# Kernel tuning notes

Hardware: AMD Instinct MI355X
Metric: run time of the kernel (lower is better)

The kernel has to match this reference:

```python
import jax, jax.numpy as jnp
import numpy as np

B, L, D = 8, 1024, 512
H, DK, DV = 8, 64, 64
DLAT = 512

def _ln(x, g, b, eps):
    m = jnp.mean(x, axis=-1, keepdims=True)
    var = jnp.mean((x - m) ** 2, axis=-1, keepdims=True)
    return (x - m) * jax.lax.rsqrt(var + eps) * g + b

def setup_inputs() -> dict:
    key = jax.random.key(0)
    ks = jax.random.split(key, 16)
    s = lambda fan: 1.0 / np.sqrt(fan)
    inp = {
        "q": jax.random.normal(ks[0], (B, L, D), jnp.float32),
        "k": jax.random.normal(ks[1], (B, L, D), jnp.float32),
        "v": jax.random.normal(ks[2], (B, L, D), jnp.float32),
        "latent": jax.random.normal(ks[3], (B, 1, DLAT), jnp.float32),
        "Wq": jax.random.normal(ks[4], (D, H * DK), jnp.float32) * s(D),
        "bq": jnp.zeros((H * DK,), jnp.float32),
        "Wk": jax.random.normal(ks[5], (D, H * DK), jnp.float32) * s(D),
        "bk": jnp.zeros((H * DK,), jnp.float32),
        "Wv": jax.random.normal(ks[6], (D, H * DV), jnp.float32) * s(D),
        "bv": jnp.zeros((H * DV,), jnp.float32),
        "Wfc": jax.random.normal(ks[7], (H * DV, D), jnp.float32) * s(H * DV),
        "bfc": jnp.zeros((D,), jnp.float32),
        "Ws1": jax.random.normal(ks[8], (DLAT, 2 * D), jnp.float32) * s(DLAT),
        "bs1": jnp.zeros((2 * D,), jnp.float32),
        "Ws2": jax.random.normal(ks[9], (D, D), jnp.float32) * s(D),
        "bs2": jnp.zeros((D,), jnp.float32),
        "en_g": jnp.ones((D,), jnp.float32),
        "en_b": jnp.zeros((D,), jnp.float32),
        "ln_g": jnp.ones((D,), jnp.float32),
        "ln_b": jnp.zeros((D,), jnp.float32),
    }
    return inp

def reference(q, k, v, latent, Wq, bq, Wk, bk, Wv, bv, Wfc, bfc, Ws1, bs1, Ws2, bs2, en_g, en_b, ln_g, ln_b):
    residual = q
    # QKV projections -> [B, L, H, d]
    Q = (q @ Wq + bq).reshape(B, L, H, DK)
    K = (k @ Wk + bk).reshape(B, L, H, DK)
    V = (v @ Wv + bv).reshape(B, L, H, DV)
    # scaled dot-product attention (dropout = identity in eval)
    scores = jnp.einsum("bqhd,bkhd->bhqk", Q, K) / jnp.sqrt(jnp.float32(DK))
    attn = jax.nn.softmax(scores, axis=-1)
    o = jnp.einsum("bhqk,bkhd->bqhd", attn, V).reshape(B, L, H * DV)
    o = o @ Wfc + bfc
    # ScaledStylizationBlock (FiLM): SiLU -> Linear -> split scale/shift
    lat = jax.nn.silu(latent) @ Ws1 + bs1          # [B, 1, 2D]
    scale, shift = jnp.split(lat, 2, axis=2)
    h = _ln(o, en_g, en_b, 1e-5) * (1.0 + scale) + shift
    h = jax.nn.silu(h) @ Ws2 + bs2
    out = _ln(h + residual, ln_g, ln_b, 1e-6)
    return out, attn
```

## Files before the change

kernel.cpp:

```cpp
#include <hip/hip_runtime.h>
#include <hip/hip_bf16.h>
#include <math.h>

#define BB 8
#define LLEN 1024
#define DDIM 512
#define HH 8
#define DLAT 512
#define NROW (BB * LLEN)
#define ROWELEM 4194304

typedef __bf16 bf16x8 __attribute__((ext_vector_type(8)));
typedef __bf16 bf16x4 __attribute__((ext_vector_type(4)));
typedef float  f32x4  __attribute__((ext_vector_type(4)));

__device__ inline __bf16 f2bf(float f) {
    union { float f; unsigned u; } a; a.f = f;
    unsigned r = (a.u + 0x7fffu + ((a.u >> 16) & 1u)) >> 16;
    union { unsigned short s; __bf16 b; } o; o.s = (unsigned short)r;
    return o.b;
}

__global__ __launch_bounds__(256) void wtrans3_kernel(
    const float* __restrict__ W0, const float* __restrict__ W1,
    const float* __restrict__ W2, __bf16* __restrict__ T0,
    __bf16* __restrict__ T1, __bf16* __restrict__ T2)
{
    const float* W = (blockIdx.y == 0) ? W0 : (blockIdx.y == 1) ? W1 : W2;
    __bf16* WT     = (blockIdx.y == 0) ? T0 : (blockIdx.y == 1) ? T1 : T2;

    __shared__ float t[64][65];
    const int tid = threadIdx.x;
    const int bx = blockIdx.x & 7;
    const int by = blockIdx.x >> 3;
    const int r0 = by * 64, c0 = bx * 64;

    #pragma unroll
    for (int p = 0; p < 4; ++p) {
        int r = p * 16 + (tid >> 4);
        int c = (tid & 15) * 4;
        f32x4 v = *(const f32x4*)(W + (size_t)(r0 + r) * 512 + c0 + c);
        t[r][c] = v[0]; t[r][c + 1] = v[1]; t[r][c + 2] = v[2]; t[r][c + 3] = v[3];
    }
    __syncthreads();
    #pragma unroll
    for (int p = 0; p < 4; ++p) {
        int c = p * 16 + (tid >> 4);
        int rc = (tid & 15) * 4;
        bf16x4 o;
        #pragma unroll
        for (int m = 0; m < 4; ++m) o[m] = f2bf(t[rc + m][c]);
        *(bf16x4*)(WT + (size_t)(c0 + c) * 512 + r0 + rc) = o;
    }
}

__global__ __launch_bounds__(256) void wtrans_hilo2_kernel(
    const float* __restrict__ W0, const float* __restrict__ W1,
    __bf16* __restrict__ H0, __bf16* __restrict__ L0,
    __bf16* __restrict__ H1, __bf16* __restrict__ L1)
{
    const float* W  = (blockIdx.y == 0) ? W0 : W1;
    __bf16* WTh     = (blockIdx.y == 0) ? H0 : H1;
    __bf16* WTl     = (blockIdx.y == 0) ? L0 : L1;

    __shared__ float t[64][65];
    const int tid = threadIdx.x;
    const int bx = blockIdx.x & 7;
    const int by = blockIdx.x >> 3;
    const int r0 = by * 64, c0 = bx * 64;

    #pragma unroll
    for (int p = 0; p < 4; ++p) {
        int r = p * 16 + (tid >> 4);
        int c = (tid & 15) * 4;
        f32x4 v = *(const f32x4*)(W + (size_t)(r0 + r) * 512 + c0 + c);
        t[r][c] = v[0]; t[r][c + 1] = v[1]; t[r][c + 2] = v[2]; t[r][c + 3] = v[3];
    }
    __syncthreads();
    #pragma unroll
    for (int p = 0; p < 4; ++p) {
        int c = p * 16 + (tid >> 4);
        int rc = (tid & 15) * 4;
        bf16x4 oh, ol;
        #pragma unroll
        for (int m = 0; m < 4; ++m) {
            float v = t[rc + m][c];
            __bf16 hi = f2bf(v);
            oh[m] = hi;
            ol[m] = f2bf(v - (float)hi);
        }
        *(bf16x4*)(WTh + (size_t)(c0 + c) * 512 + r0 + rc) = oh;
        *(bf16x4*)(WTl + (size_t)(c0 + c) * 512 + r0 + rc) = ol;
    }
}

__global__ __launch_bounds__(256) void gemm_qkv_mfma(
    const float* __restrict__ A, const __bf16* __restrict__ Bt,
    const float* __restrict__ bias, __bf16* __restrict__ C)
{
    const int tid  = threadIdx.x;
    const int w    = tid >> 6, lane = tid & 63;
    const int quad = lane >> 4, lid = lane & 15;
    const int wm = w >> 1, wn = w & 1;
    const int col0 = blockIdx.x * 64;
    const int row0 = blockIdx.y * 128;

    __shared__ __bf16 As[128][72];
    __shared__ __bf16 Bs[64][72];

    const f32x4 zero = {0.f, 0.f, 0.f, 0.f};
    f32x4 acc[4][2];
    #pragma unroll
    for (int i = 0; i < 4; ++i)
        #pragma unroll
        for (int j = 0; j < 2; ++j) acc[i][j] = zero;

    for (int kt = 0; kt < 512; kt += 64) {
        __syncthreads();
        {
            const int rr = lane >> 4;
            const int cc = lane & 15;
            #pragma unroll
            for (int p = 0; p < 8; ++p) {
                int r = w * 32 + p * 4 + rr;
                f32x4 v = *(const f32x4*)(A + (size_t)(row0 + r) * 512 + kt + cc * 4);
                bf16x4 o;
                #pragma unroll
                for (int m = 0; m < 4; ++m) o[m] = f2bf(v[m]);
                *(bf16x4*)&As[r][cc * 4] = o;
            }
        }
        {
            const int rr = lane >> 3;
            const int cc = lane & 7;
            #pragma unroll
            for (int p = 0; p < 2; ++p) {
                int r = w * 16 + p * 8 + rr;
                *(bf16x8*)&Bs[r][cc * 8] =
                    *(const bf16x8*)(Bt + (size_t)(col0 + r) * 512 + kt + cc * 8);
            }
        }
        __syncthreads();
        #pragma unroll
        for (int ks = 0; ks < 2; ++ks) {
            bf16x8 a[4], b[2];
            #pragma unroll
            for (int i = 0; i < 4; ++i)
                a[i] = *(const bf16x8*)&As[wm * 64 + i * 16 + lid][ks * 32 + quad * 8];
            #pragma unroll
            for (int j = 0; j < 2; ++j)
                b[j] = *(const bf16x8*)&Bs[wn * 32 + j * 16 + lid][ks * 32 + quad * 8];
            #pragma unroll
            for (int i = 0; i < 4; ++i)
                #pragma unroll
                for (int j = 0; j < 2; ++j)
                    acc[i][j] = __builtin_amdgcn_mfma_f32_16x16x32_bf16(a[i], b[j], acc[i][j], 0, 0, 0);
        }
    }

    float bcol[2];
    #pragma unroll
    for (int j = 0; j < 2; ++j) bcol[j] = bias[col0 + wn * 32 + j * 16 + lid];
    #pragma unroll
    for (int i = 0; i < 4; ++i)
        #pragma unroll
        for (int j = 0; j < 2; ++j) {
            int colg = col0 + wn * 32 + j * 16 + lid;
            #pragma unroll
            for (int r = 0; r < 4; ++r) {
                int rowg = row0 + wm * 64 + i * 16 + quad * 4 + r;
                C[(size_t)rowg * 512 + colg] = f2bf(acc[i][j][r] + bcol[j]);
            }
        }
}

__global__ __launch_bounds__(256) void gemm_v_mfma(
    const float* __restrict__ A, const __bf16* __restrict__ Bt,
    const float* __restrict__ bias, __bf16* __restrict__ VtG)
{
    const int tid  = threadIdx.x;
    const int w    = tid >> 6, lane = tid & 63;
    const int quad = lane >> 4, lid = lane & 15;
    const int wm = w >> 1, wn = w & 1;
    const int col0 = blockIdx.x * 64;
    const int row0 = blockIdx.y * 128;

    __shared__ __bf16 As[128][72];
    __shared__ __bf16 Bs[64][72];

    const f32x4 zero = {0.f, 0.f, 0.f, 0.f};
    f32x4 acc[4][2];
    #pragma unroll
    for (int i = 0; i < 4; ++i)
        #pragma unroll
        for (int j = 0; j < 2; ++j) acc[i][j] = zero;

    for (int kt = 0; kt < 512; kt += 64) {
        __syncthreads();
        {
            const int rr = lane >> 4;
            const int cc = lane & 15;
            #pragma unroll
            for (int p = 0; p < 8; ++p) {
                int r = w * 32 + p * 4 + rr;
                f32x4 v = *(const f32x4*)(A + (size_t)(row0 + r) * 512 + kt + cc * 4);
                bf16x4 o;
                #pragma unroll
                for (int m = 0; m < 4; ++m) o[m] = f2bf(v[m]);
                *(bf16x4*)&As[r][cc * 4] = o;
            }
        }
        {
            const int rr = lane >> 3;
            const int cc = lane & 7;
            #pragma unroll
            for (int p = 0; p < 2; ++p) {
                int r = w * 16 + p * 8 + rr;
                *(bf16x8*)&Bs[r][cc * 8] =
                    *(const bf16x8*)(Bt + (size_t)(col0 + r) * 512 + kt + cc * 8);
            }
        }
        __syncthreads();
        #pragma unroll
        for (int ks = 0; ks < 2; ++ks) {
            bf16x8 a[4], b[2];
            #pragma unroll
            for (int i = 0; i < 4; ++i)
                a[i] = *(const bf16x8*)&As[wm * 64 + i * 16 + lid][ks * 32 + quad * 8];
            #pragma unroll
            for (int j = 0; j < 2; ++j)
                b[j] = *(const bf16x8*)&Bs[wn * 32 + j * 16 + lid][ks * 32 + quad * 8];
            #pragma unroll
            for (int i = 0; i < 4; ++i)
                #pragma unroll
                for (int j = 0; j < 2; ++j)
                    acc[i][j] = __builtin_amdgcn_mfma_f32_16x16x32_bf16(a[i], b[j], acc[i][j], 0, 0, 0);
        }
    }

    __syncthreads();
    __bf16 (*Ts)[136] = (__bf16 (*)[136])(&As[0][0]);
    float bcol[2];
    #pragma unroll
    for (int j = 0; j < 2; ++j) bcol[j] = bias[col0 + wn * 32 + j * 16 + lid];
    #pragma unroll
    for (int i = 0; i < 4; ++i)
        #pragma unroll
        for (int j = 0; j < 2; ++j) {
            int d = wn * 32 + j * 16 + lid;
            #pragma unroll
            for (int r = 0; r < 4; ++r) {
                int l = wm * 64 + i * 16 + quad * 4 + r;
                Ts[d][l] = f2bf(acc[i][j][r] + bcol[j]);
            }
        }
    __syncthreads();
    const int b = row0 >> 10, l0 = row0 & 1023, h = blockIdx.x;
    const size_t obase = (size_t)((b * 8 + h) * 64) * LLEN;
    #pragma unroll
    for (int p = 0; p < 4; ++p) {
        int cix = tid + p * 256;
        int d = cix >> 4, lc = cix & 15;
        bf16x8 vv = *(const bf16x8*)&Ts[d][lc * 8];
        *(bf16x8*)(VtG + obase + (size_t)d * LLEN + l0 + lc * 8) = vv;
    }
}

__global__ __launch_bounds__(256) void gemm_split_mfma(
    const __bf16* __restrict__ Ahi, const __bf16* __restrict__ Alo,
    const __bf16* __restrict__ Bth, const __bf16* __restrict__ Btl,
    const float* __restrict__ bias, float* __restrict__ C)
{
    const int tid  = threadIdx.x;
    const int w    = tid >> 6, lane = tid & 63;
    const int quad = lane >> 4, lid = lane & 15;
    const int wm = w >> 1, wn = w & 1;
    const int col0 = blockIdx.x * 64;
    const int row0 = blockIdx.y * 128;

    __shared__ __bf16 Ah[128][40];
    __shared__ __bf16 Al[128][40];
    __shared__ __bf16 Bh[64][40];
    __shared__ __bf16 Bl[64][40];

    const f32x4 zero = {0.f, 0.f, 0.f, 0.f};
    f32x4 acc[4][2];
    #pragma unroll
    for (int i = 0; i < 4; ++i)
        #pragma unroll
        for (int j = 0; j < 2; ++j) acc[i][j] = zero;

    for (int kt = 0; kt < 512; kt += 32) {
        __syncthreads();
        #pragma unroll
        for (int p = 0; p < 2; ++p) {
            int cix = tid + p * 256;
            int r = cix >> 2, cc = cix & 3;
            size_t g = (size_t)(row0 + r) * 512 + kt + cc * 8;
            *(bf16x8*)&Ah[r][cc * 8] = *(const bf16x8*)(Ahi + g);
            *(bf16x8*)&Al[r][cc * 8] = *(const bf16x8*)(Alo + g);
        }
        {
            int r = tid >> 2, cc = tid & 3;
            size_t g = (size_t)(col0 + r) * 512 + kt + cc * 8;
            *(bf16x8*)&Bh[r][cc * 8] = *(const bf16x8*)(Bth + g);
            *(bf16x8*)&Bl[r][cc * 8] = *(const bf16x8*)(Btl + g);
        }
        __syncthreads();
        bf16x8 ah[4], al[4], bh[2], bl[2];
        #pragma unroll
        for (int i = 0; i < 4; ++i) {
            ah[i] = *(const bf16x8*)&Ah[wm * 64 + i * 16 + lid][quad * 8];
            al[i] = *(const bf16x8*)&Al[wm * 64 + i * 16 + lid][quad * 8];
        }
        #pragma unroll
        for (int j = 0; j < 2; ++j) {
            bh[j] = *(const bf16x8*)&Bh[wn * 32 + j * 16 + lid][quad * 8];
            bl[j] = *(const bf16x8*)&Bl[wn * 32 + j * 16 + lid][quad * 8];
        }
        #pragma unroll
        for (int i = 0; i < 4; ++i)
            #pragma unroll
            for (int j = 0; j < 2; ++j) {
                f32x4 t = __builtin_amdgcn_mfma_f32_16x16x32_bf16(al[i], bh[j], acc[i][j], 0, 0, 0);
                t = __builtin_amdgcn_mfma_f32_16x16x32_bf16(ah[i], bl[j], t, 0, 0, 0);
                acc[i][j] = __builtin_amdgcn_mfma_f32_16x16x32_bf16(ah[i], bh[j], t, 0, 0, 0);
            }
    }

    float bcol[2];
    #pragma unroll
    for (int j = 0; j < 2; ++j) bcol[j] = bias[col0 + wn * 32 + j * 16 + lid];
    #pragma unroll
    for (int i = 0; i < 4; ++i)
        #pragma unroll
        for (int j = 0; j < 2; ++j) {
            int colg = col0 + wn * 32 + j * 16 + lid;
            #pragma unroll
            for (int r = 0; r < 4; ++r) {
                int rowg = row0 + wm * 64 + i * 16 + quad * 4 + r;
                C[(size_t)rowg * 512 + colg] = acc[i][j][r] + bcol[j];
            }
        }
}

__global__ __launch_bounds__(256) void film_latent_kernel(
    const float* __restrict__ latent, const float* __restrict__ Ws1,
    const float* __restrict__ bs1, float* __restrict__ film)
{
    __shared__ float sl[DLAT];
    const int b = blockIdx.x;
    const int tid = threadIdx.x;
    #pragma unroll
    for (int l = 0; l < 2; ++l) {
        int k = tid + l * 256;
        float x = latent[b * DLAT + k];
        sl[k] = x / (1.f + __expf(-x));
    }
    __syncthreads();
    int n = blockIdx.y * 256 + tid;
    float acc = bs1[n];
    for (int k = 0; k < DLAT; ++k)
        acc += sl[k] * Ws1[(size_t)k * 1024 + n];
    film[b * 1024 + n] = acc;
}

__global__ __launch_bounds__(256) void attn_mfma_kernel(
    const __bf16* __restrict__ Qb, const __bf16* __restrict__ Kb,
    const __bf16* __restrict__ VtG, float* __restrict__ attn_out,
    __bf16* __restrict__ Ohi, __bf16* __restrict__ Olo)
{
    const int bid = blockIdx.x;
    const int qt = bid & 15;
    const int h  = (bid >> 4) & 7;
    const int b  = bid >> 7;
    const int q0 = qt * 64;
    const int tid = threadIdx.x;
    const int w    = tid >> 6;
    const int lane = tid & 63;
    const int quad = lane >> 4;
    const int lid  = lane & 15;

    __shared__ __bf16 KtS[2][64][72];
    __shared__ __bf16 VtS[2][64][72];
    __shared__ __bf16 PtS[4][16][72];

    const int myq = q0 + w * 16 + lid;
    const __bf16* qptr = Qb + (size_t)(b * LLEN + myq) * DDIM + h * 64 + quad * 8;
    const bf16x8 qf0 = *(const bf16x8*)(qptr);
    const bf16x8 qf1 = *(const bf16x8*)(qptr + 32);

    const size_t kbase = (size_t)(b * LLEN) * DDIM + h * 64;
    const size_t vbase = (size_t)((b * 8 + h) * 64) * LLEN;
    const f32x4 zero = {0.f, 0.f, 0.f, 0.f};
    const float C0 = 0.125f;

    const int sr = tid >> 3;
    const int sc = tid & 7;

    #pragma unroll
    for (int rep = 0; rep < 2; ++rep) {
        int r = sr + rep * 32;
        *(bf16x8*)&KtS[0][r][sc * 8] =
            *(const bf16x8*)(Kb + kbase + (size_t)r * DDIM + sc * 8);
    }
    __syncthreads();

    float rsum = 0.f;
    int cur = 0;
    for (int kt = 0; kt < 16; ++kt) {
        bf16x8 kr0, kr1;
        if (kt < 15) {
            kr0 = *(const bf16x8*)(Kb + kbase + (size_t)((kt + 1) * 64 + sr) * DDIM + sc * 8);
            kr1 = *(const bf16x8*)(Kb + kbase + (size_t)((kt + 1) * 64 + sr + 32) * DDIM + sc * 8);
        }
        #pragma unroll
        for (int st = 0; st < 4; ++st) {
            bf16x8 a0 = *(const bf16x8*)&KtS[cur][st * 16 + lid][quad * 8];
            bf16x8 a1 = *(const bf16x8*)&KtS[cur][st * 16 + lid][32 + quad * 8];
            f32x4 c = __builtin_amdgcn_mfma_f32_16x16x32_bf16(a0, qf0, zero, 0, 0, 0);
            c = __builtin_amdgcn_mfma_f32_16x16x32_bf16(a1, qf1, c, 0, 0, 0);
            #pragma unroll
            for (int r = 0; r < 4; ++r) rsum += __expf(C0 * c[r]);
        }
        if (kt < 15) {
            *(bf16x8*)&KtS[cur ^ 1][sr][sc * 8] = kr0;
            *(bf16x8*)&KtS[cur ^ 1][sr + 32][sc * 8] = kr1;
        }
        __syncthreads();
        cur ^= 1;
    }
    rsum += __shfl_xor(rsum, 16, 64);
    rsum += __shfl_xor(rsum, 32, 64);
    const float rinv = 1.f / rsum;

    f32x4 oacc[4] = {zero, zero, zero, zero};
    const size_t abase = ((size_t)((b * 8 + h) * LLEN + myq)) * LLEN;

    #pragma unroll
    for (int rep = 0; rep < 2; ++rep) {
        int r = sr + rep * 32;
        *(bf16x8*)&KtS[0][r][sc * 8] =
            *(const bf16x8*)(Kb + kbase + (size_t)r * DDIM + sc * 8);
        *(bf16x8*)&VtS[0][r][sc * 8] =
            *(const bf16x8*)(VtG + vbase + (size_t)r * LLEN + sc * 8);
    }
    __syncthreads();

    cur = 0;
    for (int kt = 0; kt < 16; ++kt) {
        bf16x8 kr0, kr1, vr0, vr1;
        if (kt < 15) {
            kr0 = *(const bf16x8*)(Kb + kbase + (size_t)((kt + 1) * 64 + sr) * DDIM + sc * 8);
            kr1 = *(const bf16x8*)(Kb + kbase + (size_t)((kt + 1) * 64 + sr + 32) * DDIM + sc * 8);
            vr0 = *(const bf16x8*)(VtG + vbase + (size_t)sr * LLEN + (kt + 1) * 64 + sc * 8);
            vr1 = *(const bf16x8*)(VtG + vbase + (size_t)(sr + 32) * LLEN + (kt + 1) * 64 + sc * 8);
        }
        #pragma unroll
        for (int st = 0; st < 4; ++st) {
            bf16x8 a0 = *(const bf16x8*)&KtS[cur][st * 16 + lid][quad * 8];
            bf16x8 a1 = *(const bf16x8*)&KtS[cur][st * 16 + lid][32 + quad * 8];
            f32x4 c = __builtin_amdgcn_mfma_f32_16x16x32_bf16(a0, qf0, zero, 0, 0, 0);
            c = __builtin_amdgcn_mfma_f32_16x16x32_bf16(a1, qf1, c, 0, 0, 0);
            f32x4 p;
            bf16x4 pk;
            #pragma unroll
            for (int r = 0; r < 4; ++r) {
                p[r] = __expf(C0 * c[r]) * rinv;
                pk[r] = f2bf(p[r]);
            }
            __builtin_nontemporal_store(p, (f32x4*)(attn_out + abase + kt * 64 + st * 16 + quad * 4));
            *(bf16x4*)&PtS[w][lid][st * 16 + quad * 4] = pk;
        }
        asm volatile("s_waitcnt lgkmcnt(0)" ::: "memory");
        #pragma unroll
        for (int kc = 0; kc < 2; ++kc) {
            bf16x8 pa = *(const bf16x8*)&PtS[w][lid][kc * 32 + quad * 8];
            #pragma unroll
            for (int nt = 0; nt < 4; ++nt) {
                bf16x8 vb = *(const bf16x8*)&VtS[cur][nt * 16 + lid][kc * 32 + quad * 8];
                oacc[nt] = __builtin_amdgcn_mfma_f32_16x16x32_bf16(pa, vb, oacc[nt], 0, 0, 0);
            }
        }
        if (kt < 15) {
            *(bf16x8*)&KtS[cur ^ 1][sr][sc * 8] = kr0;
            *(bf16x8*)&KtS[cur ^ 1][sr + 32][sc * 8] = kr1;
            *(bf16x8*)&VtS[cur ^ 1][sr][sc * 8] = vr0;
            *(bf16x8*)&VtS[cur ^ 1][sr + 32][sc * 8] = vr1;
        }
        __syncthreads();
        cur ^= 1;
    }

    #pragma unroll
    for (int nt = 0; nt < 4; ++nt)
        #pragma unroll
        for (int r = 0; r < 4; ++r) {
            float val = oacc[nt][r];
            __bf16 hi = f2bf(val);
            size_t idx = (size_t)(b * LLEN + q0 + w * 16 + quad * 4 + r) * DDIM + h * 64 + nt * 16 + lid;
            Ohi[idx] = hi;
            Olo[idx] = f2bf(val - (float)hi);
        }
}

__device__ inline void block_reduce2(float& a, float& b) {
    #pragma unroll
    for (int off = 32; off > 0; off >>= 1) {
        a += __shfl_down(a, off, 64);
        b += __shfl_down(b, off, 64);
    }
    __shared__ float wa[4], wb[4];
    int lane = threadIdx.x & 63, w = threadIdx.x >> 6;
    if (lane == 0) { wa[w] = a; wb[w] = b; }
    __syncthreads();
    if (threadIdx.x == 0) {
        wa[0] = wa[0] + wa[1] + wa[2] + wa[3];
        wb[0] = wb[0] + wb[1] + wb[2] + wb[3];
    }
    __syncthreads();
    a = wa[0];
    b = wb[0];
}

__global__ __launch_bounds__(256) void film_ln_kernel(
    const float* __restrict__ X, const float* __restrict__ en_g,
    const float* __restrict__ en_b, const float* __restrict__ film,
    __bf16* __restrict__ HShi, __bf16* __restrict__ HSlo)
{
    const int row = blockIdx.x;
    const int b = row >> 10;
    const int tid = threadIdx.x;
    const size_t base = (size_t)row * DDIM;

    float x0 = X[base + tid];
    float x1 = X[base + 256 + tid];
    float s = x0 + x1;
    float s2 = x0 * x0 + x1 * x1;
    block_reduce2(s, s2);
    float mean = s * (1.f / 512.f);
    float var = s2 * (1.f / 512.f) - mean * mean;
    float inv = rsqrtf(var + 1e-5f);

    #pragma unroll
    for (int l = 0; l < 2; ++l) {
        int d = tid + l * 256;
        float x = (l == 0) ? x0 : x1;
        float nh = (x - mean) * inv * en_g[d] + en_b[d];
        float sc = film[b * 1024 + d];
        float sh = film[b * 1024 + 512 + d];
        float hv = nh * (1.f + sc) + sh;
        float sv = hv / (1.f + __expf(-hv));
        __bf16 hi = f2bf(sv);
        HShi[base + d] = hi;
        HSlo[base + d] = f2bf(sv - (float)hi);
    }
}

__global__ __launch_bounds__(256) void final_ln_kernel(
    const float* __restrict__ H2, const float* __restrict__ resid,
    const float* __restrict__ g, const float* __restrict__ bta,
    float* __restrict__ out)
{
    const int row = blockIdx.x;
    const int tid = threadIdx.x;
    const size_t base = (size_t)row * DDIM;

    float x0 = H2[base + tid] + resid[base + tid];
    float x1 = H2[base + 256 + tid] + resid[base + 256 + tid];
    float s = x0 + x1;
    float s2 = x0 * x0 + x1 * x1;
    block_reduce2(s, s2);
    float mean = s * (1.f / 512.f);
    float var = s2 * (1.f / 512.f) - mean * mean;
    float inv = rsqrtf(var + 1e-6f);

    #pragma unroll
    for (int l = 0; l < 2; ++l) {
        int d = tid + l * 256;
        float x = (l == 0) ? x0 : x1;
        float o = (x - mean) * inv * g[d] + bta[d];
        __builtin_nontemporal_store(o, out + base + d);
    }
}

extern "C" void kernel_launch(void* const* d_in, const int* in_sizes, int n_in,
                              void* d_out, int out_size, void* d_ws, size_t ws_size,
                              hipStream_t stream)
{
    const float* q      = (const float*)d_in[0];
    const float* k      = (const float*)d_in[1];
    const float* v      = (const float*)d_in[2];
    const float* latent = (const float*)d_in[3];
    const float* Wq  = (const float*)d_in[4];
    const float* bq  = (const float*)d_in[5];
    const float* Wk  = (const float*)d_in[6];
    const float* bk  = (const float*)d_in[7];
    const float* Wv  = (const float*)d_in[8];
    const float* bv  = (const float*)d_in[9];
    const float* Wfc = (const float*)d_in[10];
    const float* bfc = (const float*)d_in[11];
    const float* Ws1 = (const float*)d_in[12];
    const float* bs1 = (const float*)d_in[13];
    const float* Ws2 = (const float*)d_in[14];
    const float* bs2 = (const float*)d_in[15];
    const float* en_g = (const float*)d_in[16];
    const float* en_b = (const float*)d_in[17];
    const float* ln_g = (const float*)d_in[18];
    const float* ln_b = (const float*)d_in[19];

    float* out  = (float*)d_out;
    float* attn = out + ROWELEM;

    char* ws = (char*)d_ws;
    __bf16* Qb   = (__bf16*)(ws + 0);
    __bf16* Kb   = (__bf16*)(ws + 8388608);
    __bf16* VtG  = (__bf16*)(ws + 16777216);
    __bf16* Ohi  = (__bf16*)(ws + 25165824);
    __bf16* Olo  = (__bf16*)(ws + 33554432);
    __bf16* WqT  = (__bf16*)(ws + 41943040);
    __bf16* WkT  = (__bf16*)(ws + 42467328);
    __bf16* WvT  = (__bf16*)(ws + 42991616);
    __bf16* WfhT = (__bf16*)(ws + 43515904);
    __bf16* WflT = (__bf16*)(ws + 44040192);
    __bf16* W2hT = (__bf16*)(ws + 44564480);
    __bf16* W2lT = (__bf16*)(ws + 45088768);
    float*  film = (float*)(ws + 45613056);

    float*  F1   = (float*)(ws + 0);
    __bf16* HShi = Ohi;
    __bf16* HSlo = Olo;
    float*  H2   = (float*)(ws + 0);

    wtrans3_kernel<<<dim3(64, 3), 256, 0, stream>>>(Wq, Wk, Wv, WqT, WkT, WvT);
    wtrans_hilo2_kernel<<<dim3(64, 2), 256, 0, stream>>>(Wfc, Ws2, WfhT, WflT, W2hT, W2lT);
    film_latent_kernel<<<dim3(BB, 4), 256, 0, stream>>>(latent, Ws1, bs1, film);

    dim3 ggrid(8, 64);
    gemm_qkv_mfma<<<ggrid, 256, 0, stream>>>(q, WqT, bq, Qb);
    gemm_qkv_mfma<<<ggrid, 256, 0, stream>>>(k, WkT, bk, Kb);
    gemm_v_mfma<<<ggrid, 256, 0, stream>>>(v, WvT, bv, VtG);

    attn_mfma_kernel<<<1024, 256, 0, stream>>>(Qb, Kb, VtG, attn, Ohi, Olo);

    gemm_split_mfma<<<ggrid, 256, 0, stream>>>(Ohi, Olo, WfhT, WflT, bfc, F1);
    film_ln_kernel<<<NROW, 256, 0, stream>>>(F1, en_g, en_b, film, HShi, HSlo);
    gemm_split_mfma<<<ggrid, 256, 0, stream>>>(HShi, HSlo, W2hT, W2lT, bs2, H2);
    final_ln_kernel<<<NROW, 256, 0, stream>>>(H2, q, ln_g, ln_b, out);
}
```

Before: 578.4 us.

## Merge weight prep and QKV GEMMs, shrink split-GEMM tiles, remap blocks across XCDs

Folds the two weight-transpose kernels into one launch and the three Q/K/V projection GEMMs into a single 1536-block launch. Halves the row tile of the hi/lo split GEMM to 64 so 1024 blocks fill the GPU. Adds an XCD-aware block index permutation (f&7 stride) to the attention, QKV and split GEMM kernels so neighbouring tiles land on the same chiplet and share L2. The intent is fewer launches, better occupancy and better cache locality, at the cost of smaller tiles with less operand reuse in the split GEMM.

```diff
diff --git a/kernel.cpp b/kernel.cpp
--- a/kernel.cpp
+++ b/kernel.cpp
@@ -21,13 +21,22 @@
     return o.b;
 }
 
-__global__ __launch_bounds__(256) void wtrans3_kernel(
-    const float* __restrict__ W0, const float* __restrict__ W1,
-    const float* __restrict__ W2, __bf16* __restrict__ T0,
-    __bf16* __restrict__ T1, __bf16* __restrict__ T2)
-{
-    const float* W = (blockIdx.y == 0) ? W0 : (blockIdx.y == 1) ? W1 : W2;
-    __bf16* WT     = (blockIdx.y == 0) ? T0 : (blockIdx.y == 1) ? T1 : T2;
+__global__ __launch_bounds__(256) void wprep_kernel(
+    const float* __restrict__ Wq, const float* __restrict__ Wk,
+    const float* __restrict__ Wv, const float* __restrict__ Wfc,
+    const float* __restrict__ Ws2,
+    __bf16* __restrict__ WqT, __bf16* __restrict__ WkT, __bf16* __restrict__ WvT,
+    __bf16* __restrict__ WfhT, __bf16* __restrict__ WflT,
+    __bf16* __restrict__ W2hT, __bf16* __restrict__ W2lT)
+{
+    const float* W; __bf16* D0; __bf16* D1 = nullptr;
+    switch (blockIdx.y) {
+        case 0: W = Wq;  D0 = WqT;  break;
+        case 1: W = Wk;  D0 = WkT;  break;
+        case 2: W = Wv;  D0 = WvT;  break;
+        case 3: W = Wfc; D0 = WfhT; D1 = WflT; break;
+        default: W = Ws2; D0 = W2hT; D1 = W2lT; break;
+    }
 
     __shared__ float t[64][65];
     const int tid = threadIdx.x;
@@ -47,63 +56,52 @@
     for (int p = 0; p < 4; ++p) {
         int c = p * 16 + (tid >> 4);
         int rc = (tid & 15) * 4;
-        bf16x4 o;
-        #pragma unroll
-        for (int m = 0; m < 4; ++m) o[m] = f2bf(t[rc + m][c]);
-        *(bf16x4*)(WT + (size_t)(c0 + c) * 512 + r0 + rc) = o;
-    }
-}
-
-__global__ __launch_bounds__(256) void wtrans_hilo2_kernel(
-    const float* __restrict__ W0, const float* __restrict__ W1,
-    __bf16* __restrict__ H0, __bf16* __restrict__ L0,
-    __bf16* __restrict__ H1, __bf16* __restrict__ L1)
-{
-    const float* W  = (blockIdx.y == 0) ? W0 : W1;
-    __bf16* WTh     = (blockIdx.y == 0) ? H0 : H1;
-    __bf16* WTl     = (blockIdx.y == 0) ? L0 : L1;
-
-    __shared__ float t[64][65];
-    const int tid = threadIdx.x;
-    const int bx = blockIdx.x & 7;
-    const int by = blockIdx.x >> 3;
-    const int r0 = by * 64, c0 = bx * 64;
-
-    #pragma unroll
-    for (int p = 0; p < 4; ++p) {
-        int r = p * 16 + (tid >> 4);
-        int c = (tid & 15) * 4;
-        f32x4 v = *(const f32x4*)(W + (size_t)(r0 + r) * 512 + c0 + c);
-        t[r][c] = v[0]; t[r][c + 1] = v[1]; t[r][c + 2] = v[2]; t[r][c + 3] = v[3];
-    }
-    __syncthreads();
-    #pragma unroll
-    for (int p = 0; p < 4; ++p) {
-        int c = p * 16 + (tid >> 4);
-        int rc = (tid & 15) * 4;
-        bf16x4 oh, ol;
-        #pragma unroll
-        for (int m = 0; m < 4; ++m) {
-            float v = t[rc + m][c];
-            __bf16 hi = f2bf(v);
-            oh[m] = hi;
-            ol[m] = f2bf(v - (float)hi);
-        }
-        *(bf16x4*)(WTh + (size_t)(c0 + c) * 512 + r0 + rc) = oh;
-        *(bf16x4*)(WTl + (size_t)(c0 + c) * 512 + r0 + rc) = ol;
-    }
-}
-
-__global__ __launch_bounds__(256) void gemm_qkv_mfma(
-    const float* __restrict__ A, const __bf16* __restrict__ Bt,
-    const float* __restrict__ bias, __bf16* __restrict__ C)
-{
+        if (D1 == nullptr) {
+            bf16x4 o;
+            #pragma unroll
+            for (int m = 0; m < 4; ++m) o[m] = f2bf(t[rc + m][c]);
+            *(bf16x4*)(D0 + (size_t)(c0 + c) * 512 + r0 + rc) = o;
+        } else {
+            bf16x4 oh, ol;
+            #pragma unroll
+            for (int m = 0; m < 4; ++m) {
+                float v = t[rc + m][c];
+                __bf16 hi = f2bf(v);
+                oh[m] = hi;
+                ol[m] = f2bf(v - (float)hi);
+            }
+            *(bf16x4*)(D0 + (size_t)(c0 + c) * 512 + r0 + rc) = oh;
+            *(bf16x4*)(D1 + (size_t)(c0 + c) * 512 + r0 + rc) = ol;
+        }
+    }
+}
+
+__global__ __launch_bounds__(256) void gemm_qkv3_mfma(
+    const float* __restrict__ q, const float* __restrict__ k,
+    const float* __restrict__ v,
+    const __bf16* __restrict__ WqT, const __bf16* __restrict__ WkT,
+    const __bf16* __restrict__ WvT,
+    const float* __restrict__ bq, const float* __restrict__ bk,
+    const float* __restrict__ bv,
+    __bf16* __restrict__ Qb, __bf16* __restrict__ Kb, __bf16* __restrict__ VtG)
+{
+    const int f = blockIdx.x;
+    const int s = (f & 7) * 192 + (f >> 3);
+    const int z   = s >> 9;
+    const int rem = s & 511;
+    const int bx  = rem & 7;
+    const int by  = rem >> 3;
+
+    const float*  A    = (z == 0) ? q   : (z == 1) ? k   : v;
+    const __bf16* Bt   = (z == 0) ? WqT : (z == 1) ? WkT : WvT;
+    const float*  bias = (z == 0) ? bq  : (z == 1) ? bk  : bv;
+
     const int tid  = threadIdx.x;
     const int w    = tid >> 6, lane = tid & 63;
     const int quad = lane >> 4, lid = lane & 15;
     const int wm = w >> 1, wn = w & 1;
-    const int col0 = blockIdx.x * 64;
-    const int row0 = blockIdx.y * 128;
+    const int col0 = bx * 64;
+    const int row0 = by * 128;
 
     __shared__ __bf16 As[128][72];
     __shared__ __bf16 Bs[64][72];
@@ -123,10 +121,10 @@
             #pragma unroll
             for (int p = 0; p < 8; ++p) {
                 int r = w * 32 + p * 4 + rr;
-                f32x4 v = *(const f32x4*)(A + (size_t)(row0 + r) * 512 + kt + cc * 4);
+                f32x4 vv = *(const f32x4*)(A + (size_t)(row0 + r) * 512 + kt + cc * 4);
                 bf16x4 o;
                 #pragma unroll
-                for (int m = 0; m < 4; ++m) o[m] = f2bf(v[m]);
+                for (int m = 0; m < 4; ++m) o[m] = f2bf(vv[m]);
                 *(bf16x4*)&As[r][cc * 4] = o;
             }
         }
@@ -161,157 +159,93 @@
     float bcol[2];
     #pragma unroll
     for (int j = 0; j < 2; ++j) bcol[j] = bias[col0 + wn * 32 + j * 16 + lid];
-    #pragma unroll
-    for (int i = 0; i < 4; ++i)
-        #pragma unroll
-        for (int j = 0; j < 2; ++j) {
-            int colg = col0 + wn * 32 + j * 16 + lid;
-            #pragma unroll
-            for (int r = 0; r < 4; ++r) {
-                int rowg = row0 + wm * 64 + i * 16 + quad * 4 + r;
-                C[(size_t)rowg * 512 + colg] = f2bf(acc[i][j][r] + bcol[j]);
-            }
-        }
-}
-
-__global__ __launch_bounds__(256) void gemm_v_mfma(
-    const float* __restrict__ A, const __bf16* __restrict__ Bt,
-    const float* __restrict__ bias, __bf16* __restrict__ VtG)
-{
+
+    if (z < 2) {
+        __bf16* C = (z == 0) ? Qb : Kb;
+        #pragma unroll
+        for (int i = 0; i < 4; ++i)
+            #pragma unroll
+            for (int j = 0; j < 2; ++j) {
+                int colg = col0 + wn * 32 + j * 16 + lid;
+                #pragma unroll
+                for (int r = 0; r < 4; ++r) {
+                    int rowg = row0 + wm * 64 + i * 16 + quad * 4 + r;
+                    C[(size_t)rowg * 512 + colg] = f2bf(acc[i][j][r] + bcol[j]);
+                }
+            }
+    } else {
+        __syncthreads();
+        __bf16 (*Ts)[136] = (__bf16 (*)[136])(&As[0][0]);
+        #pragma unroll
+        for (int i = 0; i < 4; ++i)
+            #pragma unroll
+            for (int j = 0; j < 2; ++j) {
+                int d = wn * 32 + j * 16 + lid;
+                #pragma unroll
+                for (int r = 0; r < 4; ++r) {
+                    int l = wm * 64 + i * 16 + quad * 4 + r;
+                    Ts[d][l] = f2bf(acc[i][j][r] + bcol[j]);
+                }
+            }
+        __syncthreads();
+        const int b = row0 >> 10, l0 = row0 & 1023, h = bx;
+        const size_t obase = (size_t)((b * 8 + h) * 64) * LLEN;
+        #pragma unroll
+        for (int p = 0; p < 4; ++p) {
+            int cix = tid + p * 256;
+            int d = cix >> 4, lc = cix & 15;
+            bf16x8 vv = *(const bf16x8*)&Ts[d][lc * 8];
+            *(bf16x8*)(VtG + obase + (size_t)d * LLEN + l0 + lc * 8) = vv;
+        }
+    }
+}
+
+__global__ __launch_bounds__(256) void gemm_split_mfma(
+    const __bf16* __restrict__ Ahi, const __bf16* __restrict__ Alo,
+    const __bf16* __restrict__ Bth, const __bf16* __restrict__ Btl,
+    const float* __restrict__ bias, float* __restrict__ C)
+{
+    const int f = blockIdx.x;
+    const int s = (f & 7) * 128 + (f >> 3);
+    const int bx = s & 7, by = s >> 3;
+    const int col0 = bx * 64;
+    const int row0 = by * 64;
+
     const int tid  = threadIdx.x;
     const int w    = tid >> 6, lane = tid & 63;
     const int quad = lane >> 4, lid = lane & 15;
     const int wm = w >> 1, wn = w & 1;
-    const int col0 = blockIdx.x * 64;
-    const int row0 = blockIdx.y * 128;
-
-    __shared__ __bf16 As[128][72];
-    __shared__ __bf16 Bs[64][72];
-
-    const f32x4 zero = {0.f, 0.f, 0.f, 0.f};
-    f32x4 acc[4][2];
-    #pragma unroll
-    for (int i = 0; i < 4; ++i)
-        #pragma unroll
-        for (int j = 0; j < 2; ++j) acc[i][j] = zero;
-
-    for (int kt = 0; kt < 512; kt += 64) {
-        __syncthreads();
-        {
-            const int rr = lane >> 4;
-            const int cc = lane & 15;
-            #pragma unroll
-            for (int p = 0; p < 8; ++p) {
-                int r = w * 32 + p * 4 + rr;
-                f32x4 v = *(const f32x4*)(A + (size_t)(row0 + r) * 512 + kt + cc * 4);
-                bf16x4 o;
-                #pragma unroll
-                for (int m = 0; m < 4; ++m) o[m] = f2bf(v[m]);
-                *(bf16x4*)&As[r][cc * 4] = o;
-            }
-        }
-        {
-            const int rr = lane >> 3;
-            const int cc = lane & 7;
-            #pragma unroll
-            for (int p = 0; p < 2; ++p) {
-                int r = w * 16 + p * 8 + rr;
-                *(bf16x8*)&Bs[r][cc * 8] =
-                    *(const bf16x8*)(Bt + (size_t)(col0 + r) * 512 + kt + cc * 8);
-            }
-        }
-        __syncthreads();
-        #pragma unroll
-        for (int ks = 0; ks < 2; ++ks) {
-            bf16x8 a[4], b[2];
-            #pragma unroll
-            for (int i = 0; i < 4; ++i)
-                a[i] = *(const bf16x8*)&As[wm * 64 + i * 16 + lid][ks * 32 + quad * 8];
-            #pragma unroll
-            for (int j = 0; j < 2; ++j)
-                b[j] = *(const bf16x8*)&Bs[wn * 32 + j * 16 + lid][ks * 32 + quad * 8];
-            #pragma unroll
-            for (int i = 0; i < 4; ++i)
-                #pragma unroll
-                for (int j = 0; j < 2; ++j)
-                    acc[i][j] = __builtin_amdgcn_mfma_f32_16x16x32_bf16(a[i], b[j], acc[i][j], 0, 0, 0);
-        }
-    }
-
-    __syncthreads();
-    __bf16 (*Ts)[136] = (__bf16 (*)[136])(&As[0][0]);
-    float bcol[2];
-    #pragma unroll
-    for (int j = 0; j < 2; ++j) bcol[j] = bias[col0 + wn * 32 + j * 16 + lid];
-    #pragma unroll
-    for (int i = 0; i < 4; ++i)
-        #pragma unroll
-        for (int j = 0; j < 2; ++j) {
-            int d = wn * 32 + j * 16 + lid;
-            #pragma unroll
-            for (int r = 0; r < 4; ++r) {
-                int l = wm * 64 + i * 16 + quad * 4 + r;
-                Ts[d][l] = f2bf(acc[i][j][r] + bcol[j]);
-            }
-        }
-    __syncthreads();
-    const int b = row0 >> 10, l0 = row0 & 1023, h = blockIdx.x;
-    const size_t obase = (size_t)((b * 8 + h) * 64) * LLEN;
-    #pragma unroll
-    for (int p = 0; p < 4; ++p) {
-        int cix = tid + p * 256;
-        int d = cix >> 4, lc = cix & 15;
-        bf16x8 vv = *(const bf16x8*)&Ts[d][lc * 8];
-        *(bf16x8*)(VtG + obase + (size_t)d * LLEN + l0 + lc * 8) = vv;
-    }
-}
-
-__global__ __launch_bounds__(256) void gemm_split_mfma(
-    const __bf16* __restrict__ Ahi, const __bf16* __restrict__ Alo,
-    const __bf16* __restrict__ Bth, const __bf16* __restrict__ Btl,
-    const float* __restrict__ bias, float* __restrict__ C)
-{
-    const int tid  = threadIdx.x;
-    const int w    = tid >> 6, lane = tid & 63;
-    const int quad = lane >> 4, lid = lane & 15;
-    const int wm = w >> 1, wn = w & 1;
-    const int col0 = blockIdx.x * 64;
-    const int row0 = blockIdx.y * 128;
-
-    __shared__ __bf16 Ah[128][40];
-    __shared__ __bf16 Al[128][40];
+
+    __shared__ __bf16 Ah[64][40];
+    __shared__ __bf16 Al[64][40];
     __shared__ __bf16 Bh[64][40];
     __shared__ __bf16 Bl[64][40];
 
     const f32x4 zero = {0.f, 0.f, 0.f, 0.f};
-    f32x4 acc[4][2];
-    #pragma unroll
-    for (int i = 0; i < 4; ++i)
+    f32x4 acc[2][2];
+    #pragma unroll
+    for (int i = 0; i < 2; ++i)
         #pragma unroll
         for (int j = 0; j < 2; ++j) acc[i][j] = zero;
 
+    const int rs = tid >> 2, cs = tid & 3;
+
     for (int kt = 0; kt < 512; kt += 32) {
         __syncthreads();
-        #pragma unroll
-        for (int p = 0; p < 2; ++p) {
-            int cix = tid + p * 256;
-            int r = cix >> 2, cc = cix & 3;
-            size_t g = (size_t)(row0 + r) * 512 + kt + cc * 8;
-            *(bf16x8*)&Ah[r][cc * 8] = *(const bf16x8*)(Ahi + g);
-            *(bf16x8*)&Al[r][cc * 8] = *(const bf16x8*)(Alo + g);
-        }
         {
-            int r = tid >> 2, cc = tid & 3;
-            size_t g = (size_t)(col0 + r) * 512 + kt + cc * 8;
-            *(bf16x8*)&Bh[r][cc * 8] = *(const bf16x8*)(Bth + g);
-            *(bf16x8*)&Bl[r][cc * 8] = *(const bf16x8*)(Btl + g);
-        }
-        __syncthreads();
-        bf16x8 ah[4], al[4], bh[2], bl[2];
-        #pragma unroll
-        for (int i = 0; i < 4; ++i) {
-            ah[i] = *(const bf16x8*)&Ah[wm * 64 + i * 16 + lid][quad * 8];
-            al[i] = *(const bf16x8*)&Al[wm * 64 + i * 16 + lid][quad * 8];
+            size_t ga = (size_t)(row0 + rs) * 512 + kt + cs * 8;
+            *(bf16x8*)&Ah[rs][cs * 8] = *(const bf16x8*)(Ahi + ga);
+            *(bf16x8*)&Al[rs][cs * 8] = *(const bf16x8*)(Alo + ga);
+            size_t gb = (size_t)(col0 + rs) * 512 + kt + cs * 8;
+            *(bf16x8*)&Bh[rs][cs * 8] = *(const bf16x8*)(Bth + gb);
+            *(bf16x8*)&Bl[rs][cs * 8] = *(const bf16x8*)(Btl + gb);
+        }
+        __syncthreads();
+        bf16x8 ah[2], al[2], bh[2], bl[2];
+        #pragma unroll
+        for (int i = 0; i < 2; ++i) {
+            ah[i] = *(const bf16x8*)&Ah[wm * 32 + i * 16 + lid][quad * 8];
+            al[i] = *(const bf16x8*)&Al[wm * 32 + i * 16 + lid][quad * 8];
         }
         #pragma unroll
         for (int j = 0; j < 2; ++j) {
@@ -319,7 +253,7 @@
             bl[j] = *(const bf16x8*)&Bl[wn * 32 + j * 16 + lid][quad * 8];
         }
         #pragma unroll
-        for (int i = 0; i < 4; ++i)
+        for (int i = 0; i < 2; ++i)
             #pragma unroll
             for (int j = 0; j < 2; ++j) {
                 f32x4 t = __builtin_amdgcn_mfma_f32_16x16x32_bf16(al[i], bh[j], acc[i][j], 0, 0, 0);
@@ -332,13 +266,13 @@
     #pragma unroll
     for (int j = 0; j < 2; ++j) bcol[j] = bias[col0 + wn * 32 + j * 16 + lid];
     #pragma unroll
-    for (int i = 0; i < 4; ++i)
+    for (int i = 0; i < 2; ++i)
         #pragma unroll
         for (int j = 0; j < 2; ++j) {
             int colg = col0 + wn * 32 + j * 16 + lid;
             #pragma unroll
             for (int r = 0; r < 4; ++r) {
-                int rowg = row0 + wm * 64 + i * 16 + quad * 4 + r;
+                int rowg = row0 + wm * 32 + i * 16 + quad * 4 + r;
                 C[(size_t)rowg * 512 + colg] = acc[i][j][r] + bcol[j];
             }
         }
@@ -370,7 +304,8 @@
     const __bf16* __restrict__ VtG, float* __restrict__ attn_out,
     __bf16* __restrict__ Ohi, __bf16* __restrict__ Olo)
 {
-    const int bid = blockIdx.x;
+    const int f = blockIdx.x;
+    const int bid = (f & 7) * 128 + (f >> 3);
     const int qt = bid & 15;
     const int h  = (bid >> 4) & 7;
     const int b  = bid >> 7;
@@ -632,19 +567,17 @@
     __bf16* HSlo = Olo;
     float*  H2   = (float*)(ws + 0);
 
-    wtrans3_kernel<<<dim3(64, 3), 256, 0, stream>>>(Wq, Wk, Wv, WqT, WkT, WvT);
-    wtrans_hilo2_kernel<<<dim3(64, 2), 256, 0, stream>>>(Wfc, Ws2, WfhT, WflT, W2hT, W2lT);
+    wprep_kernel<<<dim3(64, 5), 256, 0, stream>>>(
+        Wq, Wk, Wv, Wfc, Ws2, WqT, WkT, WvT, WfhT, WflT, W2hT, W2lT);
     film_latent_kernel<<<dim3(BB, 4), 256, 0, stream>>>(latent, Ws1, bs1, film);
 
-    dim3 ggrid(8, 64);
-    gemm_qkv_mfma<<<ggrid, 256, 0, stream>>>(q, WqT, bq, Qb);
-    gemm_qkv_mfma<<<ggrid, 256, 0, stream>>>(k, WkT, bk, Kb);
-    gemm_v_mfma<<<ggrid, 256, 0, stream>>>(v, WvT, bv, VtG);
+    gemm_qkv3_mfma<<<1536, 256, 0, stream>>>(
+        q, k, v, WqT, WkT, WvT, bq, bk, bv, Qb, Kb, VtG);
 
     attn_mfma_kernel<<<1024, 256, 0, stream>>>(Qb, Kb, VtG, attn, Ohi, Olo);
 
-    gemm_split_mfma<<<ggrid, 256, 0, stream>>>(Ohi, Olo, WfhT, WflT, bfc, F1);
+    gemm_split_mfma<<<1024, 256, 0, stream>>>(Ohi, Olo, WfhT, WflT, bfc, F1);
     film_ln_kernel<<<NROW, 256, 0, stream>>>(F1, en_g, en_b, film, HShi, HSlo);
-    gemm_split_mfma<<<ggrid, 256, 0, stream>>>(HShi, HSlo, W2hT, W2lT, bs2, H2);
+    gemm_split_mfma<<<1024, 256, 0, stream>>>(HShi, HSlo, W2hT, W2lT, bs2, H2);
     final_ln_kernel<<<NROW, 256, 0, stream>>>(H2, q, ln_g, ln_b, out);
 }
```

Result: faster. 531.8 us (-8.1%).
